# Kernel tuning notes

Measured on AMD Instinct MI355X. Metric: run time of the kernel, lower is better.

## Reference

```python
import jax, jax.numpy as jnp
import numpy as np

B, T, N, F_IN = 8, 288, 2000, 1
E, ID, H, K = 128, 16, 128, 20
FL = T // 2 + 1  # rfft length = in_len//2 + 1
EPS_NORM = 1e-12
EPS_LN = 1e-8


def setup_inputs() -> dict:
    key = jax.random.key(0)
    k0, k1, k2, k3, k4 = jax.random.split(key, 5)
    return {
        "x": jax.random.normal(k0, (B, T, N, F_IN), jnp.float32),
        "Ex": jax.random.normal(k1, (FL, E), jnp.float32),
        "nodes": jax.random.normal(k2, (N, ID), jnp.float32),
        "Wd": jax.random.normal(k3, (N, E + ID, H), jnp.float32),
        "Wxabs": jax.random.normal(k4, (H, H), jnp.float32),
    }


def reference(x, Ex, nodes, Wd, Wxabs):
    # [B,T,N,F] -> take feature 0 -> [B,N,T]
    xt = jnp.transpose(x[:, :, :, 0], (0, 2, 1))
    xf = jnp.abs(jnp.fft.rfft(xt, axis=-1))  # [B,N,FL]
    # F.normalize p=2 over dim=1 (nodes), then dim=2 (freq): x / max(||x||, eps)
    xf = xf / jnp.clip(jnp.sqrt(jnp.sum(xf * xf, axis=1, keepdims=True)), EPS_NORM)
    xf = xf / jnp.clip(jnp.sqrt(jnp.sum(xf * xf, axis=2, keepdims=True)), EPS_NORM)
    xe = jnp.matmul(xf, Ex)  # [B,N,E]
    # cat(): append static node identity embedding per batch element
    xk = jnp.concatenate(
        [xe, jnp.broadcast_to(nodes, (xe.shape[0], N, ID))], axis=-1
    )  # [B,N,E+ID]
    # per-node weight bmm: [N,B,E+ID] @ [N,E+ID,H] -> [B,N,H]
    x1 = jax.nn.relu(jnp.einsum('bnd,ndh->bnh', xk, Wd))
    # LayerNorm over last two dims [N,H], eps=1e-8, no affine
    mu = jnp.mean(x1, axis=(1, 2), keepdims=True)
    var = jnp.mean((x1 - mu) ** 2, axis=(1, 2), keepdims=True)
    x2 = (x1 - mu) / jnp.sqrt(var + EPS_LN)
    # dropout is identity at inference
    adp = jnp.einsum('bnh,hk->bnk', x2, Wxabs)  # convt
    adj = jnp.einsum('bnh,bmh->bnm', adp, x1)  # [B,N,N]
    adp = jax.nn.relu(adj)
    # dy_mask_graph: per-row topk over dim=2 (torch dim=1 of the [N,N] slice),
    # binary mask via scatter of ones, then elementwise mask
    _, idx = jax.lax.top_k(adp, K)  # [B,N,K]
    bi = jnp.arange(adp.shape[0])[:, None, None]
    ni = jnp.arange(N)[None, :, None]
    mask = jnp.zeros_like(adp).at[bi, ni, idx].set(1.0)
    adj_masked = adp * mask
    return jax.nn.softmax(adj_masked, axis=2)
```

## Files before the change

kernel.cpp:

```cpp
#include <hip/hip_runtime.h>
#include <math.h>

#define BB 8
#define TT 288
#define NN 2000
#define FLEN 145
#define EE 128
#define IDD 16
#define HH 128
#define DKK 144
#define KTOP 20

typedef _Float16 half8 __attribute__((ext_vector_type(8)));
typedef float f32x4 __attribute__((ext_vector_type(4)));
typedef unsigned short ushort_t;

#define OFF_TW  ((size_t)0)
#define SZ_TW   ((size_t)TT*FLEN*2)
#define OFF_XF  (OFF_TW + SZ_TW)
#define SZ_XF   ((size_t)BB*FLEN*NN)
#define OFF_ICN (OFF_XF + SZ_XF)
#define OFF_IRN (OFF_ICN + (size_t)BB*FLEN)
#define OFF_XE  (OFF_IRN + (size_t)BB*NN)
#define SZ_BNH  ((size_t)BB*NN*HH)
#define OFF_X1  (OFF_XE + SZ_BNH)
#define OFF_ADP (OFF_X1 + SZ_BNH)
#define OFF_CSW (OFF_ADP + SZ_BNH)
#define OFF_LNS (OFF_CSW + HH)
#define OFF_LNF (OFF_LNS + 16)


__device__ __forceinline__ float wredSum(float v) {
#pragma unroll
  for (int o = 32; o > 0; o >>= 1) v += __shfl_down(v, o, 64);
  return v;
}
__device__ __forceinline__ float wredSumAll(float v) {
#pragma unroll
  for (int o = 32; o > 0; o >>= 1) v += __shfl_xor(v, o, 64);
  return v;
}
__device__ __forceinline__ float wredMaxAll(float v) {
#pragma unroll
  for (int o = 32; o > 0; o >>= 1) v = fmaxf(v, __shfl_xor(v, o, 64));
  return v;
}

__device__ __forceinline__ void split16(float v, ushort_t& hi, ushort_t& lo) {
  _Float16 h = (_Float16)v;
  _Float16 l = (_Float16)(v - (float)h);
  union { _Float16 f; ushort_t u; } a, b;
  a.f = h; b.f = l;
  hi = a.u; lo = b.u;
}

__global__ void k_tw(const float* __restrict__ Wx, float* __restrict__ tw,
                     float* __restrict__ csw, float* __restrict__ lns) {
  if (blockIdx.x == 0 && threadIdx.x < 128) {
    int k = threadIdx.x;
    float s = 0.f;
    for (int h = 0; h < HH; ++h) s += Wx[h * HH + k];
    csw[k] = s;
    if (k < 16) lns[k] = 0.f;
  }
  int id = blockIdx.x * 256 + threadIdx.x;
  if (id >= TT * FLEN) return;
  int t = id / FLEN, f = id % FLEN;
  int r = (t * f) % TT;
  double th = -2.0 * 3.14159265358979323846 * (double)r / (double)TT;
  tw[2 * id]     = (float)cos(th);
  tw[2 * id + 1] = (float)sin(th);
}

__global__ void k_dft(const float* __restrict__ x, const float* __restrict__ tw,
                      float* __restrict__ xf) {
  __shared__ __align__(16) float Xs[16][128];
  __shared__ __align__(16) float TWs[16][32][2];
  const int b = blockIdx.z;
  const int f0 = blockIdx.y * 32;
  const int n0 = blockIdx.x * 128;
  const int tid = threadIdx.x;
  const int tn = tid & 31;
  const int tf = tid >> 5;
  float ar[4][4] = {}, ai[4][4] = {};
  for (int t0 = 0; t0 < TT; t0 += 16) {
    __syncthreads();
    for (int l = tid; l < 512; l += 256) {
      int row = l >> 5, q = l & 31;
      int n = n0 + q * 4;
      const float* src = x + ((size_t)b * TT + (t0 + row)) * NN + n;
      float4 v = make_float4(0, 0, 0, 0);
      if (n + 3 < NN) v = *(const float4*)src;
      else {
        if (n + 0 < NN) v.x = src[0];
        if (n + 1 < NN) v.y = src[1];
        if (n + 2 < NN) v.z = src[2];
        if (n + 3 < NN) v.w = src[3];
      }
      *(float4*)&Xs[row][q * 4] = v;
    }
    for (int l = tid; l < 512; l += 256) {
      int row = l >> 5, ff = l & 31;
      int f = f0 + ff;
      float2 cs = make_float2(0, 0);
      if (f < FLEN) cs = *(const float2*)&tw[((size_t)(t0 + row) * FLEN + f) * 2];
      *(float2*)&TWs[row][ff][0] = cs;
    }
    __syncthreads();
#pragma unroll 4
    for (int t = 0; t < 16; ++t) {
      float4 xv = *(float4*)&Xs[t][tn * 4];
      float xx[4] = {xv.x, xv.y, xv.z, xv.w};
      float4 p0 = *(float4*)&TWs[t][tf * 4][0];
      float4 p1 = *(float4*)&TWs[t][tf * 4 + 2][0];
      float c[4] = {p0.x, p0.z, p1.x, p1.z};
      float s[4] = {p0.y, p0.w, p1.y, p1.w};
#pragma unroll
      for (int i = 0; i < 4; ++i)
#pragma unroll
        for (int j = 0; j < 4; ++j) {
          ar[i][j] = fmaf(xx[j], c[i], ar[i][j]);
          ai[i][j] = fmaf(xx[j], s[i], ai[i][j]);
        }
    }
  }
#pragma unroll
  for (int i = 0; i < 4; ++i) {
    int f = f0 + tf * 4 + i;
    if (f >= FLEN) continue;
    float* dst = &xf[((size_t)b * FLEN + f) * NN];
    float o[4];
#pragma unroll
    for (int j = 0; j < 4; ++j)
      o[j] = sqrtf(ar[i][j] * ar[i][j] + ai[i][j] * ai[i][j]);
    int n = n0 + tn * 4;
    if (n + 3 < NN) *(float4*)&dst[n] = make_float4(o[0], o[1], o[2], o[3]);
    else {
#pragma unroll
      for (int j = 0; j < 4; ++j) if (n + j < NN) dst[n + j] = o[j];
    }
  }
}

__global__ void k_colnorm(const float* __restrict__ xf, float* __restrict__ icn) {
  __shared__ float sc[4];
  int bf = blockIdx.x;
  const float* rowp = xf + (size_t)bf * NN;
  float s = 0.f;
  for (int i = threadIdx.x; i < NN; i += 256) { float v = rowp[i]; s = fmaf(v, v, s); }
  s = wredSum(s);
  int lane = threadIdx.x & 63, w = threadIdx.x >> 6;
  if (lane == 0) sc[w] = s;
  __syncthreads();
  if (threadIdx.x == 0)
    icn[bf] = 1.f / fmaxf(sqrtf(sc[0] + sc[1] + sc[2] + sc[3]), 1e-12f);
}

__global__ void k_rownorm(const float* __restrict__ xf, const float* __restrict__ icn,
                          float* __restrict__ irn) {
  int b = blockIdx.y;
  int n = blockIdx.x * 256 + threadIdx.x;
  if (n >= NN) return;
  float s = 0.f;
  for (int f = 0; f < FLEN; ++f) {
    float v = xf[((size_t)b * FLEN + f) * NN + n] * icn[b * FLEN + f];
    s = fmaf(v, v, s);
  }
  irn[b * NN + n] = 1.f / fmaxf(sqrtf(s), 1e-12f);
}

__global__ void k_xe(const float* __restrict__ xf, const float* __restrict__ icn,
                     const float* __restrict__ irn, const float* __restrict__ Ex,
                     float* __restrict__ xe) {
  __shared__ __align__(16) float As[16][64];
  __shared__ __align__(16) float Bs[16][128];
  const int b = blockIdx.y;
  const int n0 = blockIdx.x * 64;
  const int tid = threadIdx.x;
  const int tn = tid >> 4, te = tid & 15;
  float acc[4][8] = {};
  for (int f0 = 0; f0 < 160; f0 += 16) {
    __syncthreads();
    {
      int kt = tid >> 4, q = tid & 15;
      int f = f0 + kt;
      int n = n0 + q * 4;
      float4 v = make_float4(0, 0, 0, 0);
      if (f < FLEN) {
        float ic = icn[b * FLEN + f];
        const float* src = &xf[((size_t)b * FLEN + f) * NN + n];
        if (n + 3 < NN) v = *(const float4*)src;
        else {
          if (n + 0 < NN) v.x = src[0];
          if (n + 1 < NN) v.y = src[1];
          if (n + 2 < NN) v.z = src[2];
          if (n + 3 < NN) v.w = src[3];
        }
        v.x *= ic; v.y *= ic; v.z *= ic; v.w *= ic;
      }
      *(float4*)&As[kt][q * 4] = v;
    }
    for (int l = tid; l < 512; l += 256) {
      int kt = l >> 5, q = l & 31;
      int f = f0 + kt;
      float4 v = make_float4(0, 0, 0, 0);
      if (f < FLEN) v = *(const float4*)&Ex[(size_t)f * EE + q * 4];
      *(float4*)&Bs[kt][q * 4] = v;
    }
    __syncthreads();
#pragma unroll
    for (int k = 0; k < 16; ++k) {
      float4 a  = *(float4*)&As[k][tn * 4];
      float4 b0 = *(float4*)&Bs[k][te * 4];
      float4 b1 = *(float4*)&Bs[k][64 + te * 4];
      float av[4] = {a.x, a.y, a.z, a.w};
      float bv[8] = {b0.x, b0.y, b0.z, b0.w, b1.x, b1.y, b1.z, b1.w};
#pragma unroll
      for (int i = 0; i < 4; ++i)
#pragma unroll
        for (int j = 0; j < 8; ++j)
          acc[i][j] = fmaf(av[i], bv[j], acc[i][j]);
    }
  }
#pragma unroll
  for (int i = 0; i < 4; ++i) {
    int n = n0 + tn * 4 + i;
    if (n >= NN) continue;
    float sc = irn[b * NN + n];
    float* dst = &xe[((size_t)b * NN + n) * EE];
    *(float4*)&dst[te * 4] =
        make_float4(acc[i][0] * sc, acc[i][1] * sc, acc[i][2] * sc, acc[i][3] * sc);
    *(float4*)&dst[64 + te * 4] =
        make_float4(acc[i][4] * sc, acc[i][5] * sc, acc[i][6] * sc, acc[i][7] * sc);
  }
}

__global__ void k_x1(const float* xe, const float* __restrict__ nodes,
                     const float* __restrict__ Wd, float* __restrict__ x1,
                     ushort_t* x1hl) {
  __shared__ __align__(16) float xk[8][DKK];
  __shared__ float red[4][32][33];
  const int n = blockIdx.x;
  const int tid = threadIdx.x;
  {
    int b = tid >> 5, q = tid & 31;
    *(float4*)&xk[b][q * 4] = *(const float4*)&xe[((size_t)b * NN + n) * EE + q * 4];
  }
  if (tid < 128) {
    int b = tid >> 4, i = tid & 15;
    xk[b][EE + i] = nodes[(size_t)n * IDD + i];
  }
  __syncthreads();
  const int h4 = tid & 31;
  const int dg = tid >> 5;
  float acc[8][4] = {};
  for (int d = dg; d < DKK; d += 8) {
    float4 wv = *(const float4*)&Wd[((size_t)n * DKK + d) * HH + h4 * 4];
#pragma unroll
    for (int b = 0; b < 8; ++b) {
      float xv = xk[b][d];
      acc[b][0] = fmaf(xv, wv.x, acc[b][0]);
      acc[b][1] = fmaf(xv, wv.y, acc[b][1]);
      acc[b][2] = fmaf(xv, wv.z, acc[b][2]);
      acc[b][3] = fmaf(xv, wv.w, acc[b][3]);
    }
  }
#pragma unroll
  for (int b = 0; b < 8; ++b)
#pragma unroll
    for (int j = 0; j < 4; ++j)
      acc[b][j] += __shfl_xor(acc[b][j], 32, 64);
  const int wv_ = tid >> 6, lane = tid & 63;
  if (lane < 32) {
#pragma unroll
    for (int b = 0; b < 8; ++b)
#pragma unroll
      for (int j = 0; j < 4; ++j)
        red[wv_][lane][b * 4 + j] = acc[b][j];
  }
  __syncthreads();
  const size_t tbase = (size_t)(n >> 4) * 4096 + (size_t)(n & 15) * 8;
#pragma unroll
  for (int o = 0; o < 4; ++o) {
    int idx = tid + o * 256;
    int b = idx >> 7, h = idx & 127;
    float s = red[0][h >> 2][b * 4 + (h & 3)] + red[1][h >> 2][b * 4 + (h & 3)] +
              red[2][h >> 2][b * 4 + (h & 3)] + red[3][h >> 2][b * 4 + (h & 3)];
    s = fmaxf(s, 0.f);
    x1[((size_t)b * NN + n) * HH + h] = s;
    ushort_t hi, lo;
    split16(s, hi, lo);
    size_t slot = (size_t)b * (125 * 4096) + tbase +
                  (size_t)((h >> 5) * 512 + ((h >> 3) & 3) * 128 + (h & 7));
    x1hl[slot] = hi;
    x1hl[slot + 2048] = lo;
  }
}

__global__ void k_ln_stats(const float* __restrict__ x1, float* __restrict__ lns) {
  __shared__ float sc[4], sc2[4];
  int b = blockIdx.y, chunk = blockIdx.x;
  const float* base = x1 + (size_t)b * NN * HH + (size_t)chunk * 8000;
  float s = 0.f, s2 = 0.f;
  for (int i = threadIdx.x; i < 8000; i += 256) {
    float v = base[i];
    s += v; s2 = fmaf(v, v, s2);
  }
  s = wredSum(s); s2 = wredSum(s2);
  int lane = threadIdx.x & 63, w = threadIdx.x >> 6;
  if (lane == 0) { sc[w] = s; sc2[w] = s2; }
  __syncthreads();
  if (threadIdx.x == 0) {
    atomicAdd(&lns[b], sc[0] + sc[1] + sc[2] + sc[3]);
    atomicAdd(&lns[8 + b], sc2[0] + sc2[1] + sc2[2] + sc2[3]);
  }
}

__global__ void k_adp(const float* __restrict__ x1, const float* __restrict__ Wx,
                      const float* __restrict__ csw, const float* __restrict__ lns,
                      ushort_t* __restrict__ adphl) {
  __shared__ __align__(16) float As[16][64];
  __shared__ __align__(16) float Bs[16][128];
  const int r0 = blockIdx.x * 64;
  const int tid = threadIdx.x;
  const int tn = tid >> 4, te = tid & 15;
  float acc[4][8] = {};
  for (int k0 = 0; k0 < HH; k0 += 16) {
    __syncthreads();
    {
      int rr = tid >> 2, kq = tid & 3;
      float4 v = *(const float4*)&x1[(size_t)(r0 + rr) * HH + k0 + kq * 4];
      As[kq * 4 + 0][rr] = v.x;
      As[kq * 4 + 1][rr] = v.y;
      As[kq * 4 + 2][rr] = v.z;
      As[kq * 4 + 3][rr] = v.w;
    }
    for (int l = tid; l < 512; l += 256) {
      int kt = l >> 5, q = l & 31;
      *(float4*)&Bs[kt][q * 4] = *(const float4*)&Wx[(size_t)(k0 + kt) * HH + q * 4];
    }
    __syncthreads();
#pragma unroll
    for (int k = 0; k < 16; ++k) {
      float4 a  = *(float4*)&As[k][tn * 4];
      float4 b0 = *(float4*)&Bs[k][te * 4];
      float4 b1 = *(float4*)&Bs[k][64 + te * 4];
      float av[4] = {a.x, a.y, a.z, a.w};
      float bv[8] = {b0.x, b0.y, b0.z, b0.w, b1.x, b1.y, b1.z, b1.w};
#pragma unroll
      for (int i = 0; i < 4; ++i)
#pragma unroll
        for (int j = 0; j < 8; ++j)
          acc[i][j] = fmaf(av[i], bv[j], acc[i][j]);
    }
  }
  float4 c0 = *(const float4*)&csw[te * 4];
  float4 c1 = *(const float4*)&csw[64 + te * 4];
  float cw[8] = {c0.x, c0.y, c0.z, c0.w, c1.x, c1.y, c1.z, c1.w};
  const int c0k = te * 4, c1k = 64 + te * 4;
  const size_t o0r = (size_t)((c0k >> 5) * 512 + ((c0k >> 3) & 3) * 128 + (c0k & 7));
  const size_t o1r = (size_t)((c1k >> 5) * 512 + ((c1k >> 3) & 3) * 128 + (c1k & 7));
#pragma unroll
  for (int i = 0; i < 4; ++i) {
    int r = r0 + tn * 4 + i;
    int b = r / NN, n = r % NN;
    float cnt = (float)(NN * HH);
    float mu = lns[b] / cnt;
    float var = fmaxf(lns[8 + b] / cnt - mu * mu, 0.f);
    float isd = 1.f / sqrtf(var + 1e-8f);
    ushort_t hi[8], lo[8];
#pragma unroll
    for (int j = 0; j < 8; ++j) {
      float o = (acc[i][j] - mu * cw[j]) * isd;
      split16(o, hi[j], lo[j]);
    }
    size_t slot = (size_t)b * (125 * 4096) + (size_t)(n >> 4) * 4096 +
                  (size_t)(n & 15) * 8;
    ushort4 u;
    u.x = hi[0]; u.y = hi[1]; u.z = hi[2]; u.w = hi[3];
    *(ushort4*)&adphl[slot + o0r] = u;
    u.x = hi[4]; u.y = hi[5]; u.z = hi[6]; u.w = hi[7];
    *(ushort4*)&adphl[slot + o1r] = u;
    u.x = lo[0]; u.y = lo[1]; u.z = lo[2]; u.w = lo[3];
    *(ushort4*)&adphl[slot + 2048 + o0r] = u;
    u.x = lo[4]; u.y = lo[5]; u.z = lo[6]; u.w = lo[7];
    *(ushort4*)&adphl[slot + 2048 + o1r] = u;
  }
}

__global__ __launch_bounds__(256, 2) void k_adjT(
    const ushort_t* __restrict__ adphl, const ushort_t* __restrict__ x1hl,
    float* __restrict__ out) {
  const int b = blockIdx.z;
  const int tA = blockIdx.y;
  const int n0 = tA * 16;
  const int tid = threadIdx.x;
  const int w = tid >> 6;
  const int lane = tid & 63;
  const int quad = lane >> 4, r16 = lane & 15;
  const int lq = quad * 128 + r16 * 8;

  half8 Ah[4], Al[4];
  {
    const ushort_t* abase = adphl + ((size_t)(b * 125 + tA)) * 4096 + lq;
#pragma unroll
    for (int ks = 0; ks < 4; ++ks) {
      Ah[ks] = *(const half8*)(abase + ks * 512);
      Al[ks] = *(const half8*)(abase + 2048 + ks * 512);
    }
  }
  const int mbase = blockIdx.x * 512 + w * 128;
  const ushort_t* Bb = x1hl + (size_t)b * (125 * 4096) + lq;
  float* obase = out + ((size_t)(b * NN + n0 + quad * 4)) * NN;

  half8 Bh0[4], Bl0[4], Bh1[4], Bl1[4];

#define LOADB(I, BH, BL)                                                      \
  {                                                                           \
    int tB_ = (mbase + (I) * 16) >> 4;                                        \
    if (tB_ > 124) tB_ = 124;         \
    const ushort_t* bb_ = Bb + (size_t)tB_ * 4096;                            \
    BH[0] = *(const half8*)(bb_);        BL[0] = *(const half8*)(bb_ + 2048); \
    BH[1] = *(const half8*)(bb_ + 512);  BL[1] = *(const half8*)(bb_ + 2560); \
    BH[2] = *(const half8*)(bb_ + 1024); BL[2] = *(const half8*)(bb_ + 3072); \
    BH[3] = *(const half8*)(bb_ + 1536); BL[3] = *(const half8*)(bb_ + 3584); \
  }

#define STEP(I, BH, BL, BH2, BL2)                                             \
  {                                                                           \
    if ((I) < 7) LOADB((I) + 1, BH2, BL2);                                    \
    __builtin_amdgcn_sched_barrier(0);      \
    f32x4 acc = (f32x4){0.f, 0.f, 0.f, 0.f};                                  \
    _Pragma("unroll")                                                         \
    for (int ks = 0; ks < 4; ++ks) {                                          \
      acc = __builtin_amdgcn_mfma_f32_16x16x32_f16(Ah[ks], BH[ks], acc, 0, 0, 0); \
      acc = __builtin_amdgcn_mfma_f32_16x16x32_f16(Ah[ks], BL[ks], acc, 0, 0, 0); \
      acc = __builtin_amdgcn_mfma_f32_16x16x32_f16(Al[ks], BH[ks], acc, 0, 0, 0); \
    }                                                                         \
    int mt_ = mbase + (I) * 16 + r16;                                         \
    if (mt_ < NN) {                                                           \
      _Pragma("unroll")                                                       \
      for (int reg = 0; reg < 4; ++reg)                                       \
        obase[(size_t)reg * NN + mt_] = fmaxf(acc[reg], 0.f);                 \
    }                                                                         \
  }

  LOADB(0, Bh0, Bl0);
  STEP(0, Bh0, Bl0, Bh1, Bl1);
  STEP(1, Bh1, Bl1, Bh0, Bl0);
  STEP(2, Bh0, Bl0, Bh1, Bl1);
  STEP(3, Bh1, Bl1, Bh0, Bl0);
  STEP(4, Bh0, Bl0, Bh1, Bl1);
  STEP(5, Bh1, Bl1, Bh0, Bl0);
  STEP(6, Bh0, Bl0, Bh1, Bl1);
  STEP(7, Bh1, Bl1, Bh0, Bl0);
#undef STEP
#undef LOADB
}

__global__ __launch_bounds__(256, 4) void k_topsm(float* out) {
  __shared__ float scrV[4][64];
  __shared__ int scrI[4][64];
  const int tid = threadIdx.x;
  const int w = tid >> 6, lane = tid & 63;
  const int r = blockIdx.x * 4 + w;
  float* g = out + (size_t)r * NN;

  f32x4 V[8];
#pragma unroll
  for (int j = 0; j < 8; ++j) {
    int m0 = j * 256 + lane * 4;
    if (m0 < NN) V[j] = *(const f32x4*)&g[m0];
    else V[j] = (f32x4){-1.f, -1.f, -1.f, -1.f};
  }

  float mx = -1.f, cp = 0.f;
#pragma unroll
  for (int j = 0; j < 8; ++j)
#pragma unroll
    for (int e = 0; e < 4; ++e) {
      mx = fmaxf(mx, V[j][e]);
      cp += (V[j][e] > 0.f) ? 1.f : 0.f;
    }
  const float m = wredMaxAll(mx);
  const float cpos = wredSumAll(cp);
  const float em = expf(-m);

  if (cpos <= 20.5f) {
    float s = 0.f;
#pragma unroll
    for (int j = 0; j < 8; ++j)
#pragma unroll
      for (int e = 0; e < 4; ++e)
        if (V[j][e] > 0.f) s += expf(V[j][e] - m);
    s = wredSumAll(s);
    const float invD = 1.f / (s + (2000.f - cpos) * em);
    const float defv = em * invD;
#pragma unroll
    for (int j = 0; j < 8; ++j) {
      int m0 = j * 256 + lane * 4;
      if (m0 >= NN) continue;
      float4 o;
      o.x = (V[j][0] > 0.f) ? expf(V[j][0] - m) * invD : defv;
      o.y = (V[j][1] > 0.f) ? expf(V[j][1] - m) * invD : defv;
      o.z = (V[j][2] > 0.f) ? expf(V[j][2] - m) * invD : defv;
      o.w = (V[j][3] > 0.f) ? expf(V[j][3] - m) * invD : defv;
      *(float4*)&g[m0] = o;
    }
  } else {
    float tval = 0.f, cf = cpos;
    if (cpos > 64.5f) {
      float tlo = 0.f, thi = m;
      bool found = false;
      for (int it = 0; it < 64 && !found; ++it) {
        float mid = (it < 12)
            ? 0.5f * (tlo + thi)
            : __uint_as_float((__float_as_uint(tlo) + __float_as_uint(thi)) >> 1);
        float c = 0.f;
#pragma unroll
        for (int j = 0; j < 8; ++j)
#pragma unroll
          for (int e = 0; e < 4; ++e)
            c += (V[j][e] > mid) ? 1.f : 0.f;
        c = wredSumAll(c);
        if (c > 64.5f) tlo = mid;
        else if (c < 19.5f) thi = mid;
        else { tval = mid; cf = c; found = true; }
      }
      if (!found) { tval = tlo; cf = 64.f; }
    }
    int cI = (int)(cf + 0.5f);
    if (cI > 64) cI = 64;

    float* sv = scrV[w];
    int* si = scrI[w];
    int base = 0;
#pragma unroll
    for (int j = 0; j < 8; ++j)
#pragma unroll
      for (int e = 0; e < 4; ++e) {
        bool p = V[j][e] > tval;
        unsigned long long msk = __ballot(p);
        if (p) {
          int pos = base + (int)__popcll(msk & ((1ull << lane) - 1ull));
          if (pos < 64) { sv[pos] = V[j][e]; si[pos] = j * 256 + lane * 4 + e; }
        }
        base += (int)__popcll(msk);
      }
    asm volatile("s_waitcnt lgkmcnt(0)" ::: "memory");

    float cv = (lane < cI) ? sv[lane] : -1.f;
    int ci = (lane < cI) ? si[lane] : 0x7fffffff;
#pragma unroll
    for (int k = 2; k <= 64; k <<= 1)
#pragma unroll
      for (int j = k >> 1; j > 0; j >>= 1) {
        float ov = __shfl_xor(cv, j, 64);
        int oi = __shfl_xor(ci, j, 64);
        bool otherBetter = (ov > cv) || (ov == cv && oi < ci);
        bool iAmLow = (lane & j) == 0;
        bool desc = (lane & k) == 0;
        bool take = (desc == iAmLow) ? otherBetter : !otherBetter;
        if (take) { cv = ov; ci = oi; }
      }
    const float t20 = __shfl(cv, 19, 64);
    float e20 = (lane < 20) ? expf(cv - m) : 0.f;
    const float s20 = wredSumAll(e20);
    const float invD = 1.f / (s20 + (2000.f - 20.f) * em);
    const float defv = em * invD;
#pragma unroll
    for (int j = 0; j < 8; ++j) {
      int m0 = j * 256 + lane * 4;
      if (m0 >= NN) continue;
      float4 o;
      o.x = (V[j][0] >= t20) ? expf(V[j][0] - m) * invD : defv;
      o.y = (V[j][1] >= t20) ? expf(V[j][1] - m) * invD : defv;
      o.z = (V[j][2] >= t20) ? expf(V[j][2] - m) * invD : defv;
      o.w = (V[j][3] >= t20) ? expf(V[j][3] - m) * invD : defv;
      *(float4*)&g[m0] = o;
    }
  }
}

extern "C" void kernel_launch(void* const* d_in, const int* in_sizes, int n_in,
                              void* d_out, int out_size, void* d_ws, size_t ws_size,
                              hipStream_t stream) {
  const float* x     = (const float*)d_in[0];
  const float* Ex    = (const float*)d_in[1];
  const float* nodes = (const float*)d_in[2];
  const float* Wd    = (const float*)d_in[3];
  const float* Wx    = (const float*)d_in[4];
  float* out = (float*)d_out;
  float* w = (float*)d_ws;
  float* tw  = w + OFF_TW;
  float* xf  = w + OFF_XF;
  float* icn = w + OFF_ICN;
  float* irn = w + OFF_IRN;
  float* xe  = w + OFF_XE;
  float* x1  = w + OFF_X1;
  float* csw = w + OFF_CSW;
  float* lns = w + OFF_LNS;
  ushort_t* adphl = (ushort_t*)(w + OFF_ADP);
  ushort_t* x1hl  = (ushort_t*)(w + OFF_XE);

  k_tw<<<(TT * FLEN + 255) / 256, 256, 0, stream>>>(Wx, tw, csw, lns);
  k_dft<<<dim3(16, 5, BB), 256, 0, stream>>>(x, tw, xf);
  k_colnorm<<<BB * FLEN, 256, 0, stream>>>(xf, icn);
  k_rownorm<<<dim3(8, BB), 256, 0, stream>>>(xf, icn, irn);
  k_xe<<<dim3(32, BB), 256, 0, stream>>>(xf, icn, irn, Ex, xe);
  k_x1<<<NN, 256, 0, stream>>>(xe, nodes, Wd, x1, x1hl);
  k_ln_stats<<<dim3(32, BB), 256, 0, stream>>>(x1, lns);
  k_adp<<<250, 256, 0, stream>>>(x1, Wx, csw, lns, adphl);
  k_adjT<<<dim3(4, 125, BB), 256, 0, stream>>>(adphl, x1hl, out);
  k_topsm<<<(BB * NN) / 4, 256, 0, stream>>>(out);
}
```

Baseline: 487.6 us.

## Enlarge DFT and adjacency register tiles; fold row-norm into xe kernel

```diff
diff --git a/kernel.cpp b/kernel.cpp
--- a/kernel.cpp
+++ b/kernel.cpp
@@ -75,14 +75,15 @@
 __global__ void k_dft(const float* __restrict__ x, const float* __restrict__ tw,
                       float* __restrict__ xf) {
   __shared__ __align__(16) float Xs[16][128];
-  __shared__ __align__(16) float TWs[16][32][2];
+  __shared__ __align__(16) float TWs[16][64][2];
   const int b = blockIdx.z;
-  const int f0 = blockIdx.y * 32;
+  const int f0 = blockIdx.y * 64;
   const int n0 = blockIdx.x * 128;
   const int tid = threadIdx.x;
-  const int tn = tid & 31;
-  const int tf = tid >> 5;
-  float ar[4][4] = {}, ai[4][4] = {};
+  const int tn = tid & 15;
+  const int tf = tid >> 4;
+  const bool fvalid = (f0 + tf * 4) < FLEN;
+  float ar[4][8] = {}, ai[4][8] = {};
   for (int t0 = 0; t0 < TT; t0 += 16) {
     __syncthreads();
     for (int l = tid; l < 512; l += 256) {
@@ -100,28 +101,38 @@
       *(float4*)&Xs[row][q * 4] = v;
     }
     for (int l = tid; l < 512; l += 256) {
-      int row = l >> 5, ff = l & 31;
-      int f = f0 + ff;
-      float2 cs = make_float2(0, 0);
-      if (f < FLEN) cs = *(const float2*)&tw[((size_t)(t0 + row) * FLEN + f) * 2];
-      *(float2*)&TWs[row][ff][0] = cs;
+      int row = l >> 5, fq = l & 31;
+      int f = f0 + fq * 2;
+      float4 v = make_float4(0, 0, 0, 0);
+      if (f < FLEN) {
+        float2 cs = *(const float2*)&tw[((size_t)(t0 + row) * FLEN + f) * 2];
+        v.x = cs.x; v.y = cs.y;
+        if (f + 1 < FLEN) {
+          float2 cs1 = *(const float2*)&tw[((size_t)(t0 + row) * FLEN + f + 1) * 2];
+          v.z = cs1.x; v.w = cs1.y;
+        }
+      }
+      *(float4*)&TWs[row][fq * 2][0] = v;
     }
     __syncthreads();
+    if (fvalid) {
 #pragma unroll 4
-    for (int t = 0; t < 16; ++t) {
-      float4 xv = *(float4*)&Xs[t][tn * 4];
-      float xx[4] = {xv.x, xv.y, xv.z, xv.w};
-      float4 p0 = *(float4*)&TWs[t][tf * 4][0];
-      float4 p1 = *(float4*)&TWs[t][tf * 4 + 2][0];
-      float c[4] = {p0.x, p0.z, p1.x, p1.z};
-      float s[4] = {p0.y, p0.w, p1.y, p1.w};
-#pragma unroll
-      for (int i = 0; i < 4; ++i)
-#pragma unroll
-        for (int j = 0; j < 4; ++j) {
-          ar[i][j] = fmaf(xx[j], c[i], ar[i][j]);
-          ai[i][j] = fmaf(xx[j], s[i], ai[i][j]);
-        }
+      for (int t = 0; t < 16; ++t) {
+        float4 xv0 = *(float4*)&Xs[t][tn * 4];
+        float4 xv1 = *(float4*)&Xs[t][64 + tn * 4];
+        float xx[8] = {xv0.x, xv0.y, xv0.z, xv0.w, xv1.x, xv1.y, xv1.z, xv1.w};
+        float4 p0 = *(float4*)&TWs[t][tf * 4][0];
+        float4 p1 = *(float4*)&TWs[t][tf * 4 + 2][0];
+        float c[4] = {p0.x, p0.z, p1.x, p1.z};
+        float s[4] = {p0.y, p0.w, p1.y, p1.w};
+#pragma unroll
+        for (int i = 0; i < 4; ++i)
+#pragma unroll
+          for (int j = 0; j < 8; ++j) {
+            ar[i][j] = fmaf(xx[j], c[i], ar[i][j]);
+            ai[i][j] = fmaf(xx[j], s[i], ai[i][j]);
+          }
+      }
     }
   }
 #pragma unroll
@@ -129,15 +140,17 @@
     int f = f0 + tf * 4 + i;
     if (f >= FLEN) continue;
     float* dst = &xf[((size_t)b * FLEN + f) * NN];
-    float o[4];
-#pragma unroll
-    for (int j = 0; j < 4; ++j)
+    float o[8];
+#pragma unroll
+    for (int j = 0; j < 8; ++j)
       o[j] = sqrtf(ar[i][j] * ar[i][j] + ai[i][j] * ai[i][j]);
     int n = n0 + tn * 4;
-    if (n + 3 < NN) *(float4*)&dst[n] = make_float4(o[0], o[1], o[2], o[3]);
+    *(float4*)&dst[n] = make_float4(o[0], o[1], o[2], o[3]);
+    int n2 = n0 + 64 + tn * 4;
+    if (n2 + 3 < NN) *(float4*)&dst[n2] = make_float4(o[4], o[5], o[6], o[7]);
     else {
 #pragma unroll
-      for (int j = 0; j < 4; ++j) if (n + j < NN) dst[n + j] = o[j];
+      for (int j = 0; j < 4; ++j) if (n2 + j < NN) dst[n2 + j] = o[j + 4];
     }
   }
 }
@@ -156,28 +169,26 @@
     icn[bf] = 1.f / fmaxf(sqrtf(sc[0] + sc[1] + sc[2] + sc[3]), 1e-12f);
 }
 
-__global__ void k_rownorm(const float* __restrict__ xf, const float* __restrict__ icn,
-                          float* __restrict__ irn) {
-  int b = blockIdx.y;
-  int n = blockIdx.x * 256 + threadIdx.x;
-  if (n >= NN) return;
-  float s = 0.f;
-  for (int f = 0; f < FLEN; ++f) {
-    float v = xf[((size_t)b * FLEN + f) * NN + n] * icn[b * FLEN + f];
-    s = fmaf(v, v, s);
-  }
-  irn[b * NN + n] = 1.f / fmaxf(sqrtf(s), 1e-12f);
-}
-
 __global__ void k_xe(const float* __restrict__ xf, const float* __restrict__ icn,
-                     const float* __restrict__ irn, const float* __restrict__ Ex,
-                     float* __restrict__ xe) {
+                     const float* __restrict__ Ex, float* __restrict__ xe) {
   __shared__ __align__(16) float As[16][64];
   __shared__ __align__(16) float Bs[16][128];
+  __shared__ float irn_s[64];
   const int b = blockIdx.y;
   const int n0 = blockIdx.x * 64;
   const int tid = threadIdx.x;
   const int tn = tid >> 4, te = tid & 15;
+  if (tid < 64) {
+    int n = n0 + tid;
+    if (n < NN) {
+      float s = 0.f;
+      for (int f = 0; f < FLEN; ++f) {
+        float v = xf[((size_t)b * FLEN + f) * NN + n] * icn[b * FLEN + f];
+        s = fmaf(v, v, s);
+      }
+      irn_s[tid] = 1.f / fmaxf(sqrtf(s), 1e-12f);
+    }
+  }
   float acc[4][8] = {};
   for (int f0 = 0; f0 < 160; f0 += 16) {
     __syncthreads();
@@ -226,7 +237,7 @@
   for (int i = 0; i < 4; ++i) {
     int n = n0 + tn * 4 + i;
     if (n >= NN) continue;
-    float sc = irn[b * NN + n];
+    float sc = irn_s[tn * 4 + i];
     float* dst = &xe[((size_t)b * NN + n) * EE];
     *(float4*)&dst[te * 4] =
         make_float4(acc[i][0] * sc, acc[i][1] * sc, acc[i][2] * sc, acc[i][3] * sc);
@@ -388,30 +399,36 @@
   }
 }
 
-__global__ __launch_bounds__(256, 2) void k_adjT(
+__global__ __launch_bounds__(256, 1) void k_adjT(
     const ushort_t* __restrict__ adphl, const ushort_t* __restrict__ x1hl,
     float* __restrict__ out) {
   const int b = blockIdx.z;
-  const int tA = blockIdx.y;
-  const int n0 = tA * 16;
+  const int tA0 = blockIdx.y * 2;
+  const int tA1 = tA0 + 1;
   const int tid = threadIdx.x;
   const int w = tid >> 6;
   const int lane = tid & 63;
   const int quad = lane >> 4, r16 = lane & 15;
   const int lq = quad * 128 + r16 * 8;
-
-  half8 Ah[4], Al[4];
+  const bool t1v = (tA1 <= 124);
+  const int tA1c = t1v ? tA1 : 124;
+
+  half8 A0h[4], A0l[4], A1h[4], A1l[4];
   {
-    const ushort_t* abase = adphl + ((size_t)(b * 125 + tA)) * 4096 + lq;
+    const ushort_t* a0 = adphl + ((size_t)(b * 125 + tA0)) * 4096 + lq;
+    const ushort_t* a1 = adphl + ((size_t)(b * 125 + tA1c)) * 4096 + lq;
 #pragma unroll
     for (int ks = 0; ks < 4; ++ks) {
-      Ah[ks] = *(const half8*)(abase + ks * 512);
-      Al[ks] = *(const half8*)(abase + 2048 + ks * 512);
+      A0h[ks] = *(const half8*)(a0 + ks * 512);
+      A0l[ks] = *(const half8*)(a0 + 2048 + ks * 512);
+      A1h[ks] = *(const half8*)(a1 + ks * 512);
+      A1l[ks] = *(const half8*)(a1 + 2048 + ks * 512);
     }
   }
   const int mbase = blockIdx.x * 512 + w * 128;
   const ushort_t* Bb = x1hl + (size_t)b * (125 * 4096) + lq;
-  float* obase = out + ((size_t)(b * NN + n0 + quad * 4)) * NN;
+  float* o0 = out + ((size_t)b * NN + tA0 * 16 + quad * 4) * NN;
+  float* o1 = out + ((size_t)b * NN + (size_t)(t1v ? tA1 * 16 : 0) + quad * 4) * NN;
 
   half8 Bh0[4], Bl0[4], Bh1[4], Bl1[4];
 
@@ -430,18 +447,27 @@
   {                                                                           \
     if ((I) < 7) LOADB((I) + 1, BH2, BL2);                                    \
     __builtin_amdgcn_sched_barrier(0);      \
-    f32x4 acc = (f32x4){0.f, 0.f, 0.f, 0.f};                                  \
+    f32x4 acc0 = (f32x4){0.f, 0.f, 0.f, 0.f};                                 \
+    f32x4 acc1 = (f32x4){0.f, 0.f, 0.f, 0.f};                                 \
     _Pragma("unroll")                                                         \
     for (int ks = 0; ks < 4; ++ks) {                                          \
-      acc = __builtin_amdgcn_mfma_f32_16x16x32_f16(Ah[ks], BH[ks], acc, 0, 0, 0); \
-      acc = __builtin_amdgcn_mfma_f32_16x16x32_f16(Ah[ks], BL[ks], acc, 0, 0, 0); \
-      acc = __builtin_amdgcn_mfma_f32_16x16x32_f16(Al[ks], BH[ks], acc, 0, 0, 0); \
+      acc0 = __builtin_amdgcn_mfma_f32_16x16x32_f16(A0h[ks], BH[ks], acc0, 0, 0, 0); \
+      acc0 = __builtin_amdgcn_mfma_f32_16x16x32_f16(A0h[ks], BL[ks], acc0, 0, 0, 0); \
+      acc0 = __builtin_amdgcn_mfma_f32_16x16x32_f16(A0l[ks], BH[ks], acc0, 0, 0, 0); \
+      acc1 = __builtin_amdgcn_mfma_f32_16x16x32_f16(A1h[ks], BH[ks], acc1, 0, 0, 0); \
+      acc1 = __builtin_amdgcn_mfma_f32_16x16x32_f16(A1h[ks], BL[ks], acc1, 0, 0, 0); \
+      acc1 = __builtin_amdgcn_mfma_f32_16x16x32_f16(A1l[ks], BH[ks], acc1, 0, 0, 0); \
     }                                                                         \
     int mt_ = mbase + (I) * 16 + r16;                                         \
     if (mt_ < NN) {                                                           \
       _Pragma("unroll")                                                       \
       for (int reg = 0; reg < 4; ++reg)                                       \
-        obase[(size_t)reg * NN + mt_] = fmaxf(acc[reg], 0.f);                 \
+        o0[(size_t)reg * NN + mt_] = fmaxf(acc0[reg], 0.f);                   \
+      if (t1v) {                                                              \
+        _Pragma("unroll")                                                     \
+        for (int reg = 0; reg < 4; ++reg)                                     \
+          o1[(size_t)reg * NN + mt_] = fmaxf(acc1[reg], 0.f);                 \
+      }                                                                       \
     }                                                                         \
   }
 
@@ -595,7 +621,6 @@
   float* tw  = w + OFF_TW;
   float* xf  = w + OFF_XF;
   float* icn = w + OFF_ICN;
-  float* irn = w + OFF_IRN;
   float* xe  = w + OFF_XE;
   float* x1  = w + OFF_X1;
   float* csw = w + OFF_CSW;
@@ -604,13 +629,12 @@
   ushort_t* x1hl  = (ushort_t*)(w + OFF_XE);
 
   k_tw<<<(TT * FLEN + 255) / 256, 256, 0, stream>>>(Wx, tw, csw, lns);
-  k_dft<<<dim3(16, 5, BB), 256, 0, stream>>>(x, tw, xf);
+  k_dft<<<dim3(16, 3, BB), 256, 0, stream>>>(x, tw, xf);
   k_colnorm<<<BB * FLEN, 256, 0, stream>>>(xf, icn);
-  k_rownorm<<<dim3(8, BB), 256, 0, stream>>>(xf, icn, irn);
-  k_xe<<<dim3(32, BB), 256, 0, stream>>>(xf, icn, irn, Ex, xe);
+  k_xe<<<dim3(32, BB), 256, 0, stream>>>(xf, icn, Ex, xe);
   k_x1<<<NN, 256, 0, stream>>>(xe, nodes, Wd, x1, x1hl);
   k_ln_stats<<<dim3(32, BB), 256, 0, stream>>>(x1, lns);
   k_adp<<<250, 256, 0, stream>>>(x1, Wx, csw, lns, adphl);
-  k_adjT<<<dim3(4, 125, BB), 256, 0, stream>>>(adphl, x1hl, out);
+  k_adjT<<<dim3(4, 63, BB), 256, 0, stream>>>(adphl, x1hl, out);
   k_topsm<<<(BB * NN) / 4, 256, 0, stream>>>(out);
 }
```

Result: no change. 482.1 us (-1.1%).
